# Kernel optimization log

Hardware: AMD Instinct MI355X
Metric: run time of the kernel (lower is better)

The kernel has to match this reference:

```python
import jax, jax.numpy as jnp
import numpy as np

T, N_NODES, B, F, K, OUT = 16, 20, 4096, 64, 3, 2
BN = B * N_NODES        # 81920 total nodes in the batched graph
E = 327680              # edges (avg degree 4)
D1, D2, D3 = F * N_NODES, (F * N_NODES) // 2, (F * N_NODES) // 4  # 1280, 640, 320


def setup_inputs() -> dict:
    key = jax.random.key(0)
    ks = jax.random.split(key, 32)
    p = lambda k, shape: (jax.random.normal(k, shape, jnp.float32) * 0.05)
    inp = {}
    inp["x_temporal"] = jax.random.normal(ks[0], (T, BN, F), jnp.float32)
    inp["edge_index"] = jax.random.randint(ks[1], (2, E), 0, BN)
    inp["edge_weight"] = jax.random.uniform(ks[2], (E,), jnp.float32)
    # GConvGRU gate ChebConvs (K Chebyshev weight matrices + bias each)
    for i, n in enumerate(["xz", "hz", "xr", "hr", "xh", "hh"]):
        inp["W_" + n] = p(ks[3 + i], (K, F, F))
        inp["b_" + n] = jnp.zeros((F,), jnp.float32)
    inp["W1"] = p(ks[10], (D1, D2)); inp["b1"] = jnp.zeros((D2,), jnp.float32)
    inp["W2"] = p(ks[11], (D2, D3)); inp["b2"] = jnp.zeros((D3,), jnp.float32)
    inp["W3"] = p(ks[12], (D3, OUT)); inp["b3"] = jnp.zeros((OUT,), jnp.float32)
    return inp


def _cheb(X, W, b, src, dst, nw):
    # ChebConv with sym normalization, lambda_max=2: L_hat = -D^-1/2 A D^-1/2
    # Tx0 = X; Tx1 = L_hat X; Tx_k = 2 L_hat Tx_{k-1} - Tx_{k-2}
    Tx0 = X
    out = Tx0 @ W[0]
    Tx1 = jax.ops.segment_sum(nw[:, None] * Tx0[src], dst, num_segments=BN)
    out = out + Tx1 @ W[1]
    for k in range(2, K):
        Tx2 = 2.0 * jax.ops.segment_sum(nw[:, None] * Tx1[src], dst, num_segments=BN) - Tx0
        out = out + Tx2 @ W[k]
        Tx0, Tx1 = Tx1, Tx2
    return out + b


def reference(x_temporal, edge_index, edge_weight,
              W_xz, b_xz, W_hz, b_hz, W_xr, b_xr, W_hr, b_hr, W_xh, b_xh, W_hh, b_hh,
              W1, b1, W2, b2, W3, b3):
    src, dst = edge_index[0], edge_index[1]
    deg = jax.ops.segment_sum(edge_weight, src, num_segments=BN)
    dinv = jnp.where(deg > 0, jax.lax.rsqrt(jnp.where(deg > 0, deg, 1.0)), 0.0)
    nw = -dinv[src] * edge_weight * dinv[dst]  # scaled-Laplacian edge weights

    def step(H, X):
        Z = jax.nn.sigmoid(_cheb(X, W_xz, b_xz, src, dst, nw) + _cheb(H, W_hz, b_hz, src, dst, nw))
        R = jax.nn.sigmoid(_cheb(X, W_xr, b_xr, src, dst, nw) + _cheb(H, W_hr, b_hr, src, dst, nw))
        Ht = jnp.tanh(_cheb(X, W_xh, b_xh, src, dst, nw) + _cheb(H * R, W_hh, b_hh, src, dst, nw))
        Hn = Z * H + (1.0 - Z) * Ht
        Hn = jax.nn.relu(Hn)  # dropout is identity in eval mode
        return Hn, None

    H0 = jnp.zeros((BN, F), x_temporal.dtype)
    H, _ = jax.lax.scan(step, H0, x_temporal)

    x = H.reshape(B, D1)                      # [B, numNodes*embed_dim]
    x = jax.nn.relu(x @ W1 + b1)
    x = jax.nn.relu(x @ W2 + b2)
    x = jax.nn.softmax(x @ W3 + b3, axis=-1)
    return x
```

## Files before the change

### kernel.cpp

```cpp
#include <hip/hip_runtime.h>
#include <hip/hip_bf16.h>
#include <math.h>

#define T_STEPS 16
#define N_NODES 20
#define BATCH 4096
#define F_DIM 64
#define BN 81920
#define E_EDGES 327680
#define D1 1280
#define D2 640
#define D3 320

typedef __attribute__((ext_vector_type(8))) short short8;
typedef __attribute__((ext_vector_type(4))) float floatx4;

static __device__ __forceinline__ float bf2f(__hip_bfloat16 v) { return __bfloat162float(v); }
static __device__ __forceinline__ float sigmoidf_(float x) { return 1.f / (1.f + expf(-x)); }
static __device__ __forceinline__ float loadf(const void* p, size_t i, int isf32) {
    return isf32 ? ((const float*)p)[i] : bf2f(((const __hip_bfloat16*)p)[i]);
}
static __device__ __forceinline__ float bflo(unsigned int u) { return __uint_as_float(u << 16); }
static __device__ __forceinline__ float bfhi(unsigned int u) { return __uint_as_float(u & 0xffff0000u); }
static __device__ __forceinline__ unsigned int f2bf_bits(float f) {
    __hip_bfloat16 b = __float2bfloat16(f);
    unsigned short us;
    __builtin_memcpy(&us, &b, 2);
    return (unsigned int)us;
}


__global__ void detect_dtype(const void* __restrict__ x, int* __restrict__ flag) {
    int lane = threadIdx.x;
    const unsigned short* u = (const unsigned short*)x;
    int bad = 0;
    for (int i = lane; i < 256; i += 64) {
        int e = (u[i] >> 7) & 0xFF;
        if (e >= 141) bad = 1;
    }
    unsigned long long m = __ballot(bad != 0);
    if (lane == 0) flag[0] = (m != 0ull) ? 1 : 0;
}

__global__ void deg_count_kernel(const int* __restrict__ ei, const void* __restrict__ ew,
                                 float* __restrict__ deg, int* __restrict__ counts,
                                 const int* __restrict__ flagp) {
    int isf32 = *flagp;
    int e = blockIdx.x * 256 + threadIdx.x;
    if (e < E_EDGES) {
        atomicAdd(&deg[ei[e]], loadf(ew, e, isf32));
        atomicAdd(&counts[ei[E_EDGES + e]], 1);
    }
}

__global__ void scan_kernel(const int* __restrict__ counts, int* __restrict__ rowptr,
                            int* __restrict__ cursor) {
    __shared__ int s[1024];
    int t = threadIdx.x;
    int base = t * 80;
    int sum = 0;
    for (int i = 0; i < 80; ++i) sum += counts[base + i];
    s[t] = sum;
    __syncthreads();
    for (int off = 1; off < 1024; off <<= 1) {
        int v = (t >= off) ? s[t - off] : 0;
        __syncthreads();
        s[t] += v;
        __syncthreads();
    }
    int run = (t > 0) ? s[t - 1] : 0;
    for (int i = 0; i < 80; ++i) {
        rowptr[base + i] = run;
        cursor[base + i] = run;
        run += counts[base + i];
    }
    if (t == 1023) rowptr[BN] = run;
}

__global__ void fill_kernel(const int* __restrict__ ei, const void* __restrict__ ew,
                            const float* __restrict__ deg,
                            int* __restrict__ cursor, int2* __restrict__ cpack,
                            const int* __restrict__ flagp) {
    int isf32 = *flagp;
    int e = blockIdx.x * 256 + threadIdx.x;
    if (e < E_EDGES) {
        int s = ei[e], d = ei[E_EDGES + e];
        float w = loadf(ew, e, isf32);
        float ds = deg[s], dd = deg[d];
        float is = (ds > 0.f) ? (1.f / sqrtf(ds)) : 0.f;
        float id = (dd > 0.f) ? (1.f / sqrtf(dd)) : 0.f;
        int p = atomicAdd(&cursor[d], 1);
        cpack[p] = make_int2(s, __float_as_int(-is * w * id));
    }
}

__global__ void prep_weights(const void* Wxz, const void* Whz,
                             const void* Wxr, const void* Whr,
                             const void* Wxh, const void* Whh,
                             const void* bxz, const void* bhz,
                             const void* bxr, const void* bhr,
                             const void* bxh, const void* bhh,
                             const void* W1, const void* b1,
                             const void* W2, const void* b2,
                             const void* W3, const void* b3,
                             __hip_bfloat16* WgT, __hip_bfloat16* WcT,
                             float* biasg, float* biasc,
                             __hip_bfloat16* W1T, float* bias1,
                             __hip_bfloat16* W2T, float* bias2,
                             float* W3f, float* b3f, const int* __restrict__ flagp) {
    int isf32 = *flagp;
    int tid = blockIdx.x * 256 + threadIdx.x;
    if (tid < 73728) {
        int n = tid / 384, kk = tid - (tid / 384) * 384;
        int m = kk >> 6, jj = kk & 63;
        int grp = n >> 6, cc = n & 63;
        const void* Wx = (grp == 0) ? Wxz : ((grp == 1) ? Wxr : Wxh);
        const void* Wh = (grp == 0) ? Whz : ((grp == 1) ? Whr : nullptr);
        int ch = m & 1;
        int ti = m >> 1;
        const void* W = ch ? Wh : Wx;
        float v = 0.f;
        int o = jj * 64 + cc;
        if (W) {
            if (ti == 0)      v = loadf(W, o, isf32) - loadf(W, 2 * 4096 + o, isf32);
            else if (ti == 1) v = loadf(W, 4096 + o, isf32);
            else              v = 2.f * loadf(W, 2 * 4096 + o, isf32);
        }
        WgT[tid] = __float2bfloat16(v);
    } else if (tid < 86016) {
        int t2 = tid - 73728;
        int n = t2 / 192, kk = t2 - (t2 / 192) * 192;
        int m = kk >> 6, jj = kk & 63;
        int o = jj * 64 + n;
        float v;
        if (m == 0)      v = loadf(Whh, o, isf32) - loadf(Whh, 2 * 4096 + o, isf32);
        else if (m == 1) v = loadf(Whh, 4096 + o, isf32);
        else             v = 2.f * loadf(Whh, 2 * 4096 + o, isf32);
        WcT[t2] = __float2bfloat16(v);
    } else if (tid < 86208) {
        int c = tid - 86016;
        int grp = c >> 6, cc = c & 63;
        float v = (grp == 0) ? (loadf(bxz, cc, isf32) + loadf(bhz, cc, isf32))
                 : (grp == 1) ? (loadf(bxr, cc, isf32) + loadf(bhr, cc, isf32))
                              : loadf(bxh, cc, isf32);
        biasg[c] = v;
    } else if (tid < 86272) {
        biasc[tid - 86208] = loadf(bhh, tid - 86208, isf32);
    } else if (tid < 86912) {
        bias1[tid - 86272] = loadf(b1, tid - 86272, isf32);
    } else if (tid < 87232) {
        bias2[tid - 86912] = loadf(b2, tid - 86912, isf32);
    } else if (tid < 87872) {
        W3f[tid - 87232] = loadf(W3, tid - 87232, isf32);
    } else if (tid < 87874) {
        b3f[tid - 87872] = loadf(b3, tid - 87872, isf32);
    } else if (tid < 907074) {
        int t = tid - 87874;
        int n = t / 1280, k = t - (t / 1280) * 1280;
        W1T[t] = __float2bfloat16(loadf(W1, (size_t)k * 640 + n, isf32));
    } else if (tid < 1111874) {
        int t = tid - 907074;
        int n = t / 640, k = t - (t / 640) * 640;
        W2T[t] = __float2bfloat16(loadf(W2, (size_t)k * 320 + n, isf32));
    }
}

__global__ void init_x_kernel(const void* __restrict__ x, const int* __restrict__ flagp,
                              __hip_bfloat16* __restrict__ A6) {
    int isf32 = *flagp;
    int idx = blockIdx.x * 256 + threadIdx.x;
    int r = idx >> 6, c = idx & 63;
    A6[(size_t)r * 384 + c] = __float2bfloat16(loadf(x, idx, isf32));
}

__global__ void phase_pair_kernel(const int* __restrict__ rowptr, const int2* __restrict__ cpack,
                                  __hip_bfloat16* __restrict__ A6, int in_boff, int out_boff) {
    int row = __builtin_amdgcn_readfirstlane(blockIdx.x * 4 + (threadIdx.x >> 6));
    int lane = threadIdx.x & 63;
    int e0 = rowptr[row], e1 = rowptr[row + 1];
    const char* base = (const char*)A6 + in_boff;
    int boff = lane * 4;
    float ax = 0.f, ay = 0.f, bx = 0.f, by = 0.f;
    int e = e0;
    for (; e + 2 <= e1; e += 2) {
        int2 c0 = cpack[e], c1 = cpack[e + 1];
        unsigned int u0 = *(const unsigned int*)(base + (size_t)c0.x * 768 + boff);
        unsigned int u1 = *(const unsigned int*)(base + (size_t)c1.x * 768 + boff);
        float v0 = __int_as_float(c0.y), v1 = __int_as_float(c1.y);
        ax = fmaf(v0, bflo(u0), ax); ay = fmaf(v0, bfhi(u0), ay);
        bx = fmaf(v1, bflo(u1), bx); by = fmaf(v1, bfhi(u1), by);
    }
    if (e < e1) {
        int2 c0 = cpack[e];
        unsigned int u0 = *(const unsigned int*)(base + (size_t)c0.x * 768 + boff);
        float v0 = __int_as_float(c0.y);
        ax = fmaf(v0, bflo(u0), ax); ay = fmaf(v0, bfhi(u0), ay);
    }
    ax += bx; ay += by;
    unsigned int pk = f2bf_bits(ax) | (f2bf_bits(ay) << 16);
    *(unsigned int*)((char*)A6 + (size_t)row * 768 + out_boff +
                     ((lane >> 5) << 7) + ((lane & 31) << 2)) = pk;
}

__global__ void spmm_pair_kernel(const int* __restrict__ rowptr, const int2* __restrict__ cpack,
                                 __hip_bfloat16* __restrict__ Gbuf, int in_boff, int out_boff) {
    int lane = threadIdx.x & 63;
    int half = lane >> 5, lh = lane & 31;
    int row = (blockIdx.x * 4 + (threadIdx.x >> 6)) * 2 + half;
    int e0 = rowptr[row], e1 = rowptr[row + 1];
    const char* base = (const char*)Gbuf + in_boff;
    int boff = lh * 4;
    float ax = 0.f, ay = 0.f, bx = 0.f, by = 0.f;
    int e = e0;
    for (; e + 2 <= e1; e += 2) {
        int2 c0 = cpack[e], c1 = cpack[e + 1];
        unsigned int u0 = *(const unsigned int*)(base + (size_t)c0.x * 384 + boff);
        unsigned int u1 = *(const unsigned int*)(base + (size_t)c1.x * 384 + boff);
        float v0 = __int_as_float(c0.y), v1 = __int_as_float(c1.y);
        ax = fmaf(v0, bflo(u0), ax); ay = fmaf(v0, bfhi(u0), ay);
        bx = fmaf(v1, bflo(u1), bx); by = fmaf(v1, bfhi(u1), by);
    }
    if (e < e1) {
        int2 c0 = cpack[e];
        unsigned int u0 = *(const unsigned int*)(base + (size_t)c0.x * 384 + boff);
        float v0 = __int_as_float(c0.y);
        ax = fmaf(v0, bflo(u0), ax); ay = fmaf(v0, bfhi(u0), ay);
    }
    ax += bx; ay += by;
    unsigned int pk = f2bf_bits(ax) | (f2bf_bits(ay) << 16);
    *(unsigned int*)((char*)Gbuf + (size_t)row * 384 + out_boff + boff) = pk;
}

template <int MW, int NT, int EPI>
__launch_bounds__(256)
__global__ void mfma_gemm(const __hip_bfloat16* __restrict__ A, int lda,
                          const __hip_bfloat16* __restrict__ WT, int ldk,
                          const float* __restrict__ bias, int K,
                          float* __restrict__ Zbuf, float* __restrict__ hxbuf,
                          float* __restrict__ Hf, __hip_bfloat16* A6,
                          __hip_bfloat16* __restrict__ Gbuf,
                          __hip_bfloat16* __restrict__ C, int ldc,
                          const void* __restrict__ xsrc, unsigned long long xoff,
                          const int* __restrict__ flagp,
                          __hip_bfloat16* __restrict__ Hdout) {
    int wave = threadIdx.x >> 6;
    int lane = threadIdx.x & 63;
    int l15 = lane & 15, quad = lane >> 4;
    int m0 = blockIdx.x * (MW * 64) + wave * (MW * 16);
    int n0 = blockIdx.y * (NT * 16);
    int isf32 = 0;
    if (EPI == 2 && flagp) isf32 = *flagp;

    floatx4 acc[MW][NT];
#pragma unroll
    for (int mi = 0; mi < MW; ++mi)
#pragma unroll
        for (int nt = 0; nt < NT; ++nt) acc[mi][nt] = (floatx4){0.f, 0.f, 0.f, 0.f};

    for (int k0 = 0; k0 < K; k0 += 32) {
        short8 a[MW];
#pragma unroll
        for (int mi = 0; mi < MW; ++mi)
            a[mi] = *(const short8*)(A + (size_t)(m0 + mi * 16 + l15) * lda + k0 + quad * 8);
#pragma unroll
        for (int nt = 0; nt < NT; ++nt) {
            short8 b = *(const short8*)(WT + (size_t)(n0 + nt * 16 + l15) * ldk + k0 + quad * 8);
#pragma unroll
            for (int mi = 0; mi < MW; ++mi)
                acc[mi][nt] = __builtin_amdgcn_mfma_f32_16x16x32_bf16(a[mi], b, acc[mi][nt], 0, 0, 0);
        }
    }

#pragma unroll
    for (int mi = 0; mi < MW; ++mi)
#pragma unroll
        for (int nt = 0; nt < NT; ++nt) {
            int cl = n0 + nt * 16 + l15;
#pragma unroll
            for (int reg = 0; reg < 4; ++reg) {
                int r = m0 + mi * 16 + quad * 4 + reg;
                float v = acc[mi][nt][reg];
                if (EPI == 0) {
                    C[(size_t)r * ldc + cl] = __float2bfloat16(fmaxf(v + bias[cl], 0.f));
                } else if (EPI == 1) {
                    v += bias[cl];
                    if (cl < 64) {
                        Zbuf[(size_t)r * 64 + cl] = sigmoidf_(v);
                    } else if (cl < 128) {
                        int cc = cl - 64;
                        float g = sigmoidf_(v) * Hf[(size_t)r * 64 + cc];
                        Gbuf[(size_t)r * 192 + cc] = __float2bfloat16(g);
                    } else {
                        int cc = cl - 128;
                        hxbuf[(size_t)r * 64 + cc] = v;
                    }
                } else {
                    float pre = v + bias[cl] + hxbuf[(size_t)r * 64 + cl];
                    float ht = tanhf(pre);
                    float z = Zbuf[(size_t)r * 64 + cl];
                    float h = Hf[(size_t)r * 64 + cl];
                    float hn = fmaxf(z * h + (1.f - z) * ht, 0.f);
                    __hip_bfloat16 hb = __float2bfloat16(hn);
                    if (xsrc) {
                        Hf[(size_t)r * 64 + cl] = hn;
                        A6[(size_t)r * 384 + 64 + cl] = hb;
                        A6[(size_t)r * 384 + cl] =
                            __float2bfloat16(loadf(xsrc, xoff + (size_t)r * 64 + cl, isf32));
                    } else {
                        Hdout[(size_t)r * 64 + cl] = hb;
                    }
                }
            }
        }
}

__global__ void mlp3_kernel(const __hip_bfloat16* __restrict__ h2, const float* __restrict__ W3f,
                            const float* __restrict__ b3f, void* __restrict__ out,
                            const int* __restrict__ flagp) {
    int isf32 = *flagp;
    int b = blockIdx.x * 4 + (threadIdx.x >> 6);
    int lane = threadIdx.x & 63;
    float a0 = 0.f, a1 = 0.f;
    for (int k = lane; k < D3; k += 64) {
        float h = bf2f(h2[(size_t)b * D3 + k]);
        a0 = fmaf(h, W3f[k * 2 + 0], a0);
        a1 = fmaf(h, W3f[k * 2 + 1], a1);
    }
    for (int off = 32; off; off >>= 1) {
        a0 += __shfl_down(a0, off, 64);
        a1 += __shfl_down(a1, off, 64);
    }
    if (lane == 0) {
        a0 += b3f[0];
        a1 += b3f[1];
        float m = fmaxf(a0, a1);
        float e0 = expf(a0 - m), e1 = expf(a1 - m);
        float s = e0 + e1;
        if (isf32) {
            ((float*)out)[b * 2 + 0] = e0 / s;
            ((float*)out)[b * 2 + 1] = e1 / s;
        } else {
            ((__hip_bfloat16*)out)[b * 2 + 0] = __float2bfloat16(e0 / s);
            ((__hip_bfloat16*)out)[b * 2 + 1] = __float2bfloat16(e1 / s);
        }
    }
}

extern "C" void kernel_launch(void* const* d_in, const int* in_sizes, int n_in,
                              void* d_out, int out_size, void* d_ws, size_t ws_size,
                              hipStream_t stream) {
    const void* x   = d_in[0];
    const int*  ei  = (const int*)d_in[1];
    const void* ew  = d_in[2];
    const void* Wxz = d_in[3];
    const void* bxz = d_in[4];
    const void* Whz = d_in[5];
    const void* bhz = d_in[6];
    const void* Wxr = d_in[7];
    const void* bxr = d_in[8];
    const void* Whr = d_in[9];
    const void* bhr = d_in[10];
    const void* Wxh = d_in[11];
    const void* bxh = d_in[12];
    const void* Whh = d_in[13];
    const void* bhh = d_in[14];
    const void* W1  = d_in[15];
    const void* b1  = d_in[16];
    const void* W2  = d_in[17];
    const void* b2  = d_in[18];
    const void* W3  = d_in[19];
    const void* b3  = d_in[20];

    char* ws = (char*)d_ws;
    size_t off = 0;
    auto alloc = [&](size_t bytes) { char* p = ws + off; off += (bytes + 255) & ~(size_t)255; return p; };
    __hip_bfloat16* A6  = (__hip_bfloat16*)alloc((size_t)BN * 384 * 2);
    __hip_bfloat16* Gbuf = (__hip_bfloat16*)alloc((size_t)BN * 192 * 2);
    float* Hf    = (float*)alloc((size_t)BN * 64 * 4);
    float* Zbuf  = (float*)alloc((size_t)BN * 64 * 4);
    float* hxbuf = (float*)alloc((size_t)BN * 64 * 4);
    __hip_bfloat16* Hd  = (__hip_bfloat16*)alloc((size_t)BN * 64 * 2);
    __hip_bfloat16* h1  = (__hip_bfloat16*)alloc((size_t)BATCH * D2 * 2);
    __hip_bfloat16* h2  = (__hip_bfloat16*)alloc((size_t)BATCH * D3 * 2);
    float* deg    = (float*)alloc((size_t)BN * 4);
    int*   counts = (int*)alloc((size_t)BN * 4);
    int*   rowptr = (int*)alloc((size_t)(BN + 1) * 4);
    int*   cursor = (int*)alloc((size_t)BN * 4);
    int2*  cpack  = (int2*)alloc((size_t)E_EDGES * 8);
    __hip_bfloat16* WgT = (__hip_bfloat16*)alloc(192 * 384 * 2);
    __hip_bfloat16* WcT = (__hip_bfloat16*)alloc(64 * 192 * 2);
    float* biasg  = (float*)alloc(192 * 4);
    float* biasc  = (float*)alloc(64 * 4);
    __hip_bfloat16* W1T = (__hip_bfloat16*)alloc((size_t)D2 * D1 * 2);
    float* bias1  = (float*)alloc(D2 * 4);
    __hip_bfloat16* W2T = (__hip_bfloat16*)alloc((size_t)D3 * D2 * 2);
    float* bias2  = (float*)alloc(D3 * 4);
    float* W3f    = (float*)alloc(D3 * 2 * 4);
    float* b3f    = (float*)alloc(2 * 4);
    int*   flag   = (int*)alloc(256);
    (void)ws_size; (void)in_sizes; (void)n_in; (void)out_size;

    hipMemsetAsync(A6, 0, (size_t)BN * 384 * 2, stream);
    hipMemsetAsync(Hf, 0, (size_t)BN * 64 * 4, stream);
    hipMemsetAsync(deg, 0, (size_t)BN * 4, stream);
    hipMemsetAsync(counts, 0, (size_t)BN * 4, stream);

    detect_dtype<<<1, 64, 0, stream>>>(x, flag);

    const int EB = E_EDGES / 256;
    deg_count_kernel<<<EB, 256, 0, stream>>>(ei, ew, deg, counts, flag);
    scan_kernel<<<1, 1024, 0, stream>>>(counts, rowptr, cursor);
    fill_kernel<<<EB, 256, 0, stream>>>(ei, ew, deg, cursor, cpack, flag);
    prep_weights<<<4344, 256, 0, stream>>>(Wxz, Whz, Wxr, Whr, Wxh, Whh,
                                           bxz, bhz, bxr, bhr, bxh, bhh,
                                           W1, b1, W2, b2, W3, b3,
                                           WgT, WcT, biasg, biasc,
                                           W1T, bias1, W2T, bias2, W3f, b3f, flag);
    init_x_kernel<<<(BN * 64) / 256, 256, 0, stream>>>(x, flag, A6);

    const int RB = BN / 4;
    const int RB2 = BN / 8;
    for (int t = 0; t < T_STEPS; ++t) {
        phase_pair_kernel<<<RB, 256, 0, stream>>>(rowptr, cpack, A6, 0, 256);
        phase_pair_kernel<<<RB, 256, 0, stream>>>(rowptr, cpack, A6, 256, 512);
        mfma_gemm<2, 6, 1><<<dim3(BN / 128, 2), 256, 0, stream>>>(
            A6, 384, WgT, 384, biasg, 384, Zbuf, hxbuf, Hf, A6, Gbuf, nullptr, 0,
            nullptr, 0ull, nullptr, nullptr);
        spmm_pair_kernel<<<RB2, 256, 0, stream>>>(rowptr, cpack, Gbuf, 0, 128);
        spmm_pair_kernel<<<RB2, 256, 0, stream>>>(rowptr, cpack, Gbuf, 128, 256);
        const void* xn = (t + 1 < T_STEPS) ? x : nullptr;
        unsigned long long xo = (unsigned long long)(t + 1) * BN * 64;
        mfma_gemm<2, 2, 2><<<dim3(BN / 128, 2), 256, 0, stream>>>(
            Gbuf, 192, WcT, 192, biasc, 192, Zbuf, hxbuf, Hf, A6, Gbuf, nullptr, 0,
            xn, xo, flag, Hd);
    }

    mfma_gemm<1, 4, 0><<<dim3(BATCH / 64, D2 / 64), 256, 0, stream>>>(
        Hd, D1, W1T, D1, bias1, D1, nullptr, nullptr, nullptr, nullptr, nullptr, h1, D2,
        nullptr, 0ull, nullptr, nullptr);
    mfma_gemm<1, 4, 0><<<dim3(BATCH / 64, D3 / 64), 256, 0, stream>>>(
        h1, D2, W2T, D2, bias2, D2, nullptr, nullptr, nullptr, nullptr, nullptr, h2, D3,
        nullptr, 0ull, nullptr, nullptr);
    mlp3_kernel<<<BATCH / 4, 256, 0, stream>>>(h2, W3f, b3f, d_out, flag);
}
```

Measured before the change: 4.042 ms.

## Fuse second Chebyshev SpMM hop into gate and candidate GEMM kernels via LDS

The second SpMM hop of each Chebyshev recurrence is moved into the gate and candidate GEMM kernels. Each block gathers its 128 rows of neighbour features into shared memory, then runs the MFMA GEMM with those rows as the final K slice. This drops the third A6 slice and Gbuf slice from global memory, narrows row strides from 768/384 to 512/256 bytes, and removes two kernel launches per timestep. The gather loops are also unrolled to four edges. In exchange the fused blocks do their sparse gather serially per wave before the GEMM, with a full GEMM column width of 12 tiles per block, which may cost occupancy and latency hiding.

Result: slower. 6.124 ms (+51.5%).

```diff
diff --git a/kernel.cpp b/kernel.cpp
--- a/kernel.cpp
+++ b/kernel.cpp
@@ -170,148 +170,310 @@
     int isf32 = *flagp;
     int idx = blockIdx.x * 256 + threadIdx.x;
     int r = idx >> 6, c = idx & 63;
-    A6[(size_t)r * 384 + c] = __float2bfloat16(loadf(x, idx, isf32));
-}
-
-__global__ void phase_pair_kernel(const int* __restrict__ rowptr, const int2* __restrict__ cpack,
-                                  __hip_bfloat16* __restrict__ A6, int in_boff, int out_boff) {
+    A6[(size_t)r * 256 + c] = __float2bfloat16(loadf(x, idx, isf32));
+}
+
+__global__ void phaseA_kernel(const int* __restrict__ rowptr, const int2* __restrict__ cpack,
+                              __hip_bfloat16* __restrict__ A6) {
     int row = __builtin_amdgcn_readfirstlane(blockIdx.x * 4 + (threadIdx.x >> 6));
     int lane = threadIdx.x & 63;
     int e0 = rowptr[row], e1 = rowptr[row + 1];
-    const char* base = (const char*)A6 + in_boff;
+    const char* base = (const char*)A6;
     int boff = lane * 4;
-    float ax = 0.f, ay = 0.f, bx = 0.f, by = 0.f;
+    float ax = 0.f, ay = 0.f, cx = 0.f, cy = 0.f;
     int e = e0;
-    for (; e + 2 <= e1; e += 2) {
-        int2 c0 = cpack[e], c1 = cpack[e + 1];
-        unsigned int u0 = *(const unsigned int*)(base + (size_t)c0.x * 768 + boff);
-        unsigned int u1 = *(const unsigned int*)(base + (size_t)c1.x * 768 + boff);
+    for (; e + 4 <= e1; e += 4) {
+        int2 c0 = cpack[e], c1 = cpack[e + 1], c2 = cpack[e + 2], c3 = cpack[e + 3];
+        unsigned int u0 = *(const unsigned int*)(base + (size_t)c0.x * 512 + boff);
+        unsigned int u1 = *(const unsigned int*)(base + (size_t)c1.x * 512 + boff);
+        unsigned int u2 = *(const unsigned int*)(base + (size_t)c2.x * 512 + boff);
+        unsigned int u3 = *(const unsigned int*)(base + (size_t)c3.x * 512 + boff);
         float v0 = __int_as_float(c0.y), v1 = __int_as_float(c1.y);
+        float v2 = __int_as_float(c2.y), v3 = __int_as_float(c3.y);
         ax = fmaf(v0, bflo(u0), ax); ay = fmaf(v0, bfhi(u0), ay);
-        bx = fmaf(v1, bflo(u1), bx); by = fmaf(v1, bfhi(u1), by);
-    }
-    if (e < e1) {
+        cx = fmaf(v1, bflo(u1), cx); cy = fmaf(v1, bfhi(u1), cy);
+        ax = fmaf(v2, bflo(u2), ax); ay = fmaf(v2, bfhi(u2), ay);
+        cx = fmaf(v3, bflo(u3), cx); cy = fmaf(v3, bfhi(u3), cy);
+    }
+    for (; e < e1; ++e) {
         int2 c0 = cpack[e];
-        unsigned int u0 = *(const unsigned int*)(base + (size_t)c0.x * 768 + boff);
+        unsigned int u0 = *(const unsigned int*)(base + (size_t)c0.x * 512 + boff);
         float v0 = __int_as_float(c0.y);
         ax = fmaf(v0, bflo(u0), ax); ay = fmaf(v0, bfhi(u0), ay);
     }
-    ax += bx; ay += by;
+    ax += cx; ay += cy;
     unsigned int pk = f2bf_bits(ax) | (f2bf_bits(ay) << 16);
-    *(unsigned int*)((char*)A6 + (size_t)row * 768 + out_boff +
-                     ((lane >> 5) << 7) + ((lane & 31) << 2)) = pk;
+    *(unsigned int*)((char*)A6 + (size_t)row * 512 + 256 + boff) = pk;
 }
 
 __global__ void spmm_pair_kernel(const int* __restrict__ rowptr, const int2* __restrict__ cpack,
-                                 __hip_bfloat16* __restrict__ Gbuf, int in_boff, int out_boff) {
+                                 __hip_bfloat16* __restrict__ Gbuf) {
     int lane = threadIdx.x & 63;
     int half = lane >> 5, lh = lane & 31;
     int row = (blockIdx.x * 4 + (threadIdx.x >> 6)) * 2 + half;
     int e0 = rowptr[row], e1 = rowptr[row + 1];
-    const char* base = (const char*)Gbuf + in_boff;
+    const char* base = (const char*)Gbuf;
     int boff = lh * 4;
-    float ax = 0.f, ay = 0.f, bx = 0.f, by = 0.f;
+    float ax = 0.f, ay = 0.f, cx = 0.f, cy = 0.f;
     int e = e0;
-    for (; e + 2 <= e1; e += 2) {
-        int2 c0 = cpack[e], c1 = cpack[e + 1];
-        unsigned int u0 = *(const unsigned int*)(base + (size_t)c0.x * 384 + boff);
-        unsigned int u1 = *(const unsigned int*)(base + (size_t)c1.x * 384 + boff);
+    for (; e + 4 <= e1; e += 4) {
+        int2 c0 = cpack[e], c1 = cpack[e + 1], c2 = cpack[e + 2], c3 = cpack[e + 3];
+        unsigned int u0 = *(const unsigned int*)(base + (size_t)c0.x * 256 + boff);
+        unsigned int u1 = *(const unsigned int*)(base + (size_t)c1.x * 256 + boff);
+        unsigned int u2 = *(const unsigned int*)(base + (size_t)c2.x * 256 + boff);
+        unsigned int u3 = *(const unsigned int*)(base + (size_t)c3.x * 256 + boff);
         float v0 = __int_as_float(c0.y), v1 = __int_as_float(c1.y);
+        float v2 = __int_as_float(c2.y), v3 = __int_as_float(c3.y);
         ax = fmaf(v0, bflo(u0), ax); ay = fmaf(v0, bfhi(u0), ay);
-        bx = fmaf(v1, bflo(u1), bx); by = fmaf(v1, bfhi(u1), by);
-    }
-    if (e < e1) {
+        cx = fmaf(v1, bflo(u1), cx); cy = fmaf(v1, bfhi(u1), cy);
+        ax = fmaf(v2, bflo(u2), ax); ay = fmaf(v2, bfhi(u2), ay);
+        cx = fmaf(v3, bflo(u3), cx); cy = fmaf(v3, bfhi(u3), cy);
+    }
+    for (; e < e1; ++e) {
         int2 c0 = cpack[e];
-        unsigned int u0 = *(const unsigned int*)(base + (size_t)c0.x * 384 + boff);
+        unsigned int u0 = *(const unsigned int*)(base + (size_t)c0.x * 256 + boff);
         float v0 = __int_as_float(c0.y);
         ax = fmaf(v0, bflo(u0), ax); ay = fmaf(v0, bfhi(u0), ay);
     }
-    ax += bx; ay += by;
+    ax += cx; ay += cy;
     unsigned int pk = f2bf_bits(ax) | (f2bf_bits(ay) << 16);
-    *(unsigned int*)((char*)Gbuf + (size_t)row * 384 + out_boff + boff) = pk;
-}
-
-template <int MW, int NT, int EPI>
+    *(unsigned int*)((char*)Gbuf + (size_t)row * 256 + 128 + boff) = pk;
+}
+
 __launch_bounds__(256)
-__global__ void mfma_gemm(const __hip_bfloat16* __restrict__ A, int lda,
-                          const __hip_bfloat16* __restrict__ WT, int ldk,
-                          const float* __restrict__ bias, int K,
-                          float* __restrict__ Zbuf, float* __restrict__ hxbuf,
-                          float* __restrict__ Hf, __hip_bfloat16* A6,
-                          __hip_bfloat16* __restrict__ Gbuf,
-                          __hip_bfloat16* __restrict__ C, int ldc,
-                          const void* __restrict__ xsrc, unsigned long long xoff,
-                          const int* __restrict__ flagp,
-                          __hip_bfloat16* __restrict__ Hdout) {
+__global__ void fused_gates_kernel(const int* __restrict__ rowptr, const int2* __restrict__ cpack,
+                                   const __hip_bfloat16* __restrict__ A6,
+                                   const __hip_bfloat16* __restrict__ WgT,
+                                   const float* __restrict__ biasg,
+                                   const float* __restrict__ Hf,
+                                   float* __restrict__ Zbuf, float* __restrict__ hxbuf,
+                                   __hip_bfloat16* __restrict__ Gbuf) {
+    __shared__ unsigned int sX2H2[128 * 68];
+    int wave = threadIdx.x >> 6, lane = threadIdx.x & 63;
+    int l15 = lane & 15, quad = lane >> 4;
+    int r0 = blockIdx.x * 128;
+    const char* gbase = (const char*)A6 + 256;
+    int boff = lane * 4;
+    for (int i = 0; i < 32; ++i) {
+        int lr = wave * 32 + i;
+        int row = r0 + lr;
+        int e0 = rowptr[row], e1 = rowptr[row + 1];
+        float ax = 0.f, ay = 0.f, cx = 0.f, cy = 0.f;
+        int e = e0;
+        for (; e + 4 <= e1; e += 4) {
+            int2 c0 = cpack[e], c1 = cpack[e + 1], c2 = cpack[e + 2], c3 = cpack[e + 3];
+            unsigned int u0 = *(const unsigned int*)(gbase + (size_t)c0.x * 512 + boff);
+            unsigned int u1 = *(const unsigned int*)(gbase + (size_t)c1.x * 512 + boff);
+            unsigned int u2 = *(const unsigned int*)(gbase + (size_t)c2.x * 512 + boff);
+            unsigned int u3 = *(const unsigned int*)(gbase + (size_t)c3.x * 512 + boff);
+            float v0 = __int_as_float(c0.y), v1 = __int_as_float(c1.y);
+            float v2 = __int_as_float(c2.y), v3 = __int_as_float(c3.y);
+            ax = fmaf(v0, bflo(u0), ax); ay = fmaf(v0, bfhi(u0), ay);
+            cx = fmaf(v1, bflo(u1), cx); cy = fmaf(v1, bfhi(u1), cy);
+            ax = fmaf(v2, bflo(u2), ax); ay = fmaf(v2, bfhi(u2), ay);
+            cx = fmaf(v3, bflo(u3), cx); cy = fmaf(v3, bfhi(u3), cy);
+        }
+        for (; e < e1; ++e) {
+            int2 c0 = cpack[e];
+            unsigned int u0 = *(const unsigned int*)(gbase + (size_t)c0.x * 512 + boff);
+            float v0 = __int_as_float(c0.y);
+            ax = fmaf(v0, bflo(u0), ax); ay = fmaf(v0, bfhi(u0), ay);
+        }
+        ax += cx; ay += cy;
+        sX2H2[lr * 68 + lane] = f2bf_bits(ax) | (f2bf_bits(ay) << 16);
+    }
+    __syncthreads();
+
+    floatx4 acc[2][12];
+#pragma unroll
+    for (int mi = 0; mi < 2; ++mi)
+#pragma unroll
+        for (int nt = 0; nt < 12; ++nt) acc[mi][nt] = (floatx4){0.f, 0.f, 0.f, 0.f};
+
+#pragma unroll
+    for (int k0 = 0; k0 < 384; k0 += 32) {
+        short8 a[2];
+        if (k0 < 256) {
+#pragma unroll
+            for (int mi = 0; mi < 2; ++mi)
+                a[mi] = *(const short8*)(A6 + (size_t)(r0 + wave * 32 + mi * 16 + l15) * 256
+                                         + k0 + quad * 8);
+        } else {
+#pragma unroll
+            for (int mi = 0; mi < 2; ++mi)
+                a[mi] = *(const short8*)((const char*)sX2H2
+                                         + (wave * 32 + mi * 16 + l15) * 272
+                                         + (k0 - 256) * 2 + quad * 16);
+        }
+#pragma unroll
+        for (int nt = 0; nt < 12; ++nt) {
+            short8 b = *(const short8*)(WgT + (size_t)(nt * 16 + l15) * 384 + k0 + quad * 8);
+#pragma unroll
+            for (int mi = 0; mi < 2; ++mi)
+                acc[mi][nt] = __builtin_amdgcn_mfma_f32_16x16x32_bf16(a[mi], b, acc[mi][nt], 0, 0, 0);
+        }
+    }
+
+#pragma unroll
+    for (int mi = 0; mi < 2; ++mi)
+#pragma unroll
+        for (int nt = 0; nt < 12; ++nt) {
+            int cl = nt * 16 + l15;
+#pragma unroll
+            for (int reg = 0; reg < 4; ++reg) {
+                int r = r0 + wave * 32 + mi * 16 + quad * 4 + reg;
+                float v = acc[mi][nt][reg] + biasg[cl];
+                if (cl < 64) {
+                    Zbuf[(size_t)r * 64 + cl] = sigmoidf_(v);
+                } else if (cl < 128) {
+                    int cc = cl - 64;
+                    float g = sigmoidf_(v) * Hf[(size_t)r * 64 + cc];
+                    Gbuf[(size_t)r * 128 + cc] = __float2bfloat16(g);
+                } else {
+                    hxbuf[(size_t)r * 64 + (cl - 128)] = v;
+                }
+            }
+        }
+}
+
+__launch_bounds__(256)
+__global__ void fused_cand_kernel(const int* __restrict__ rowptr, const int2* __restrict__ cpack,
+                                  const __hip_bfloat16* __restrict__ Gbuf,
+                                  const __hip_bfloat16* __restrict__ WcT,
+                                  const float* __restrict__ biasc,
+                                  const float* __restrict__ Zbuf,
+                                  const float* __restrict__ hxbuf,
+                                  float* __restrict__ Hf, __hip_bfloat16* __restrict__ A6,
+                                  const void* __restrict__ xsrc, unsigned long long xoff,
+                                  const int* __restrict__ flagp,
+                                  __hip_bfloat16* __restrict__ Hdout) {
+    __shared__ unsigned int sG2[128 * 36];
+    int wave = threadIdx.x >> 6, lane = threadIdx.x & 63;
+    int l15 = lane & 15, quad = lane >> 4;
+    int half = lane >> 5, lh = lane & 31;
+    int r0 = blockIdx.x * 128;
+    int isf32 = *flagp;
+    const char* gbase = (const char*)Gbuf + 128;
+    int boff = lh * 4;
+    for (int i = 0; i < 32; i += 2) {
+        int lr = wave * 32 + i + half;
+        int row = r0 + lr;
+        int e0 = rowptr[row], e1 = rowptr[row + 1];
+        float ax = 0.f, ay = 0.f, cx = 0.f, cy = 0.f;
+        int e = e0;
+        for (; e + 4 <= e1; e += 4) {
+            int2 c0 = cpack[e], c1 = cpack[e + 1], c2 = cpack[e + 2], c3 = cpack[e + 3];
+            unsigned int u0 = *(const unsigned int*)(gbase + (size_t)c0.x * 256 + boff);
+            unsigned int u1 = *(const unsigned int*)(gbase + (size_t)c1.x * 256 + boff);
+            unsigned int u2 = *(const unsigned int*)(gbase + (size_t)c2.x * 256 + boff);
+            unsigned int u3 = *(const unsigned int*)(gbase + (size_t)c3.x * 256 + boff);
+            float v0 = __int_as_float(c0.y), v1 = __int_as_float(c1.y);
+            float v2 = __int_as_float(c2.y), v3 = __int_as_float(c3.y);
+            ax = fmaf(v0, bflo(u0), ax); ay = fmaf(v0, bfhi(u0), ay);
+            cx = fmaf(v1, bflo(u1), cx); cy = fmaf(v1, bfhi(u1), cy);
+            ax = fmaf(v2, bflo(u2), ax); ay = fmaf(v2, bfhi(u2), ay);
+            cx = fmaf(v3, bflo(u3), cx); cy = fmaf(v3, bfhi(u3), cy);
+        }
+        for (; e < e1; ++e) {
+            int2 c0 = cpack[e];
+            unsigned int u0 = *(const unsigned int*)(gbase + (size_t)c0.x * 256 + boff);
+            float v0 = __int_as_float(c0.y);
+            ax = fmaf(v0, bflo(u0), ax); ay = fmaf(v0, bfhi(u0), ay);
+        }
+        ax += cx; ay += cy;
+        sG2[lr * 36 + lh] = f2bf_bits(ax) | (f2bf_bits(ay) << 16);
+    }
+    __syncthreads();
+
+    floatx4 acc[2][4];
+#pragma unroll
+    for (int mi = 0; mi < 2; ++mi)
+#pragma unroll
+        for (int nt = 0; nt < 4; ++nt) acc[mi][nt] = (floatx4){0.f, 0.f, 0.f, 0.f};
+
+#pragma unroll
+    for (int k0 = 0; k0 < 192; k0 += 32) {
+        short8 a[2];
+        if (k0 < 128) {
+#pragma unroll
+            for (int mi = 0; mi < 2; ++mi)
+                a[mi] = *(const short8*)(Gbuf + (size_t)(r0 + wave * 32 + mi * 16 + l15) * 128
+                                         + k0 + quad * 8);
+        } else {
+#pragma unroll
+            for (int mi = 0; mi < 2; ++mi)
+                a[mi] = *(const short8*)((const char*)sG2
+                                         + (wave * 32 + mi * 16 + l15) * 144
+                                         + (k0 - 128) * 2 + quad * 16);
+        }
+#pragma unroll
+        for (int nt = 0; nt < 4; ++nt) {
+            short8 b = *(const short8*)(WcT + (size_t)(nt * 16 + l15) * 192 + k0 + quad * 8);
+#pragma unroll
+            for (int mi = 0; mi < 2; ++mi)
+                acc[mi][nt] = __builtin_amdgcn_mfma_f32_16x16x32_bf16(a[mi], b, acc[mi][nt], 0, 0, 0);
+        }
+    }
+
+#pragma unroll
+    for (int mi = 0; mi < 2; ++mi)
+#pragma unroll
+        for (int nt = 0; nt < 4; ++nt) {
+            int cl = nt * 16 + l15;
+#pragma unroll
+            for (int reg = 0; reg < 4; ++reg) {
+                int r = r0 + wave * 32 + mi * 16 + quad * 4 + reg;
+                float pre = acc[mi][nt][reg] + biasc[cl] + hxbuf[(size_t)r * 64 + cl];
+                float ht = tanhf(pre);
+                float z = Zbuf[(size_t)r * 64 + cl];
+                float h = Hf[(size_t)r * 64 + cl];
+                float hn = fmaxf(z * h + (1.f - z) * ht, 0.f);
+                __hip_bfloat16 hb = __float2bfloat16(hn);
+                if (xsrc) {
+                    Hf[(size_t)r * 64 + cl] = hn;
+                    A6[(size_t)r * 256 + 64 + cl] = hb;
+                    A6[(size_t)r * 256 + cl] =
+                        __float2bfloat16(loadf(xsrc, xoff + (size_t)r * 64 + cl, isf32));
+                } else {
+                    Hdout[(size_t)r * 64 + cl] = hb;
+                }
+            }
+        }
+}
+
+template <int NT>
+__launch_bounds__(256)
+__global__ void mfma_gemm_relu(const __hip_bfloat16* __restrict__ A, int lda,
+                               const __hip_bfloat16* __restrict__ WT,
+                               const float* __restrict__ bias, int K,
+                               __hip_bfloat16* __restrict__ C, int ldc) {
     int wave = threadIdx.x >> 6;
     int lane = threadIdx.x & 63;
     int l15 = lane & 15, quad = lane >> 4;
-    int m0 = blockIdx.x * (MW * 64) + wave * (MW * 16);
+    int m0 = blockIdx.x * 64 + wave * 16;
     int n0 = blockIdx.y * (NT * 16);
-    int isf32 = 0;
-    if (EPI == 2 && flagp) isf32 = *flagp;
-
-    floatx4 acc[MW][NT];
-#pragma unroll
-    for (int mi = 0; mi < MW; ++mi)
-#pragma unroll
-        for (int nt = 0; nt < NT; ++nt) acc[mi][nt] = (floatx4){0.f, 0.f, 0.f, 0.f};
+
+    floatx4 acc[NT];
+#pragma unroll
+    for (int nt = 0; nt < NT; ++nt) acc[nt] = (floatx4){0.f, 0.f, 0.f, 0.f};
 
     for (int k0 = 0; k0 < K; k0 += 32) {
-        short8 a[MW];
-#pragma unroll
-        for (int mi = 0; mi < MW; ++mi)
-            a[mi] = *(const short8*)(A + (size_t)(m0 + mi * 16 + l15) * lda + k0 + quad * 8);
+        short8 a = *(const short8*)(A + (size_t)(m0 + l15) * lda + k0 + quad * 8);
 #pragma unroll
         for (int nt = 0; nt < NT; ++nt) {
-            short8 b = *(const short8*)(WT + (size_t)(n0 + nt * 16 + l15) * ldk + k0 + quad * 8);
-#pragma unroll
-            for (int mi = 0; mi < MW; ++mi)
-                acc[mi][nt] = __builtin_amdgcn_mfma_f32_16x16x32_bf16(a[mi], b, acc[mi][nt], 0, 0, 0);
-        }
-    }
-
-#pragma unroll
-    for (int mi = 0; mi < MW; ++mi)
-#pragma unroll
-        for (int nt = 0; nt < NT; ++nt) {
-            int cl = n0 + nt * 16 + l15;
-#pragma unroll
-            for (int reg = 0; reg < 4; ++reg) {
-                int r = m0 + mi * 16 + quad * 4 + reg;
-                float v = acc[mi][nt][reg];
-                if (EPI == 0) {
-                    C[(size_t)r * ldc + cl] = __float2bfloat16(fmaxf(v + bias[cl], 0.f));
-                } else if (EPI == 1) {
-                    v += bias[cl];
-                    if (cl < 64) {
-                        Zbuf[(size_t)r * 64 + cl] = sigmoidf_(v);
-                    } else if (cl < 128) {
-                        int cc = cl - 64;
-                        float g = sigmoidf_(v) * Hf[(size_t)r * 64 + cc];
-                        Gbuf[(size_t)r * 192 + cc] = __float2bfloat16(g);
-                    } else {
-                        int cc = cl - 128;
-                        hxbuf[(size_t)r * 64 + cc] = v;
-                    }
-                } else {
-                    float pre = v + bias[cl] + hxbuf[(size_t)r * 64 + cl];
-                    float ht = tanhf(pre);
-                    float z = Zbuf[(size_t)r * 64 + cl];
-                    float h = Hf[(size_t)r * 64 + cl];
-                    float hn = fmaxf(z * h + (1.f - z) * ht, 0.f);
-                    __hip_bfloat16 hb = __float2bfloat16(hn);
-                    if (xsrc) {
-                        Hf[(size_t)r * 64 + cl] = hn;
-                        A6[(size_t)r * 384 + 64 + cl] = hb;
-                        A6[(size_t)r * 384 + cl] =
-                            __float2bfloat16(loadf(xsrc, xoff + (size_t)r * 64 + cl, isf32));
-                    } else {
-                        Hdout[(size_t)r * 64 + cl] = hb;
-                    }
-                }
-            }
-        }
+            short8 b = *(const short8*)(WT + (size_t)(n0 + nt * 16 + l15) * lda + k0 + quad * 8);
+            acc[nt] = __builtin_amdgcn_mfma_f32_16x16x32_bf16(a, b, acc[nt], 0, 0, 0);
+        }
+    }
+#pragma unroll
+    for (int nt = 0; nt < NT; ++nt) {
+        int cl = n0 + nt * 16 + l15;
+#pragma unroll
+        for (int reg = 0; reg < 4; ++reg) {
+            int r = m0 + quad * 4 + reg;
+            C[(size_t)r * ldc + cl] = __float2bfloat16(fmaxf(acc[nt][reg] + bias[cl], 0.f));
+        }
+    }
 }
 
 __global__ void mlp3_kernel(const __hip_bfloat16* __restrict__ h2, const float* __restrict__ W3f,
@@ -374,8 +536,8 @@
     char* ws = (char*)d_ws;
     size_t off = 0;
     auto alloc = [&](size_t bytes) { char* p = ws + off; off += (bytes + 255) & ~(size_t)255; return p; };
-    __hip_bfloat16* A6  = (__hip_bfloat16*)alloc((size_t)BN * 384 * 2);
-    __hip_bfloat16* Gbuf = (__hip_bfloat16*)alloc((size_t)BN * 192 * 2);
+    __hip_bfloat16* A6   = (__hip_bfloat16*)alloc((size_t)BN * 256 * 2);
+    __hip_bfloat16* Gbuf = (__hip_bfloat16*)alloc((size_t)BN * 128 * 2);
     float* Hf    = (float*)alloc((size_t)BN * 64 * 4);
     float* Zbuf  = (float*)alloc((size_t)BN * 64 * 4);
     float* hxbuf = (float*)alloc((size_t)BN * 64 * 4);
@@ -400,7 +562,7 @@
     int*   flag   = (int*)alloc(256);
     (void)ws_size; (void)in_sizes; (void)n_in; (void)out_size;
 
-    hipMemsetAsync(A6, 0, (size_t)BN * 384 * 2, stream);
+    hipMemsetAsync(A6, 0, (size_t)BN * 256 * 2, stream);
     hipMemsetAsync(Hf, 0, (size_t)BN * 64 * 4, stream);
     hipMemsetAsync(deg, 0, (size_t)BN * 4, stream);
     hipMemsetAsync(counts, 0, (size_t)BN * 4, stream);
@@ -420,26 +582,21 @@
 
     const int RB = BN / 4;
     const int RB2 = BN / 8;
+    const int FB = BN / 128;
     for (int t = 0; t < T_STEPS; ++t) {
-        phase_pair_kernel<<<RB, 256, 0, stream>>>(rowptr, cpack, A6, 0, 256);
-        phase_pair_kernel<<<RB, 256, 0, stream>>>(rowptr, cpack, A6, 256, 512);
-        mfma_gemm<2, 6, 1><<<dim3(BN / 128, 2), 256, 0, stream>>>(
-            A6, 384, WgT, 384, biasg, 384, Zbuf, hxbuf, Hf, A6, Gbuf, nullptr, 0,
-            nullptr, 0ull, nullptr, nullptr);
-        spmm_pair_kernel<<<RB2, 256, 0, stream>>>(rowptr, cpack, Gbuf, 0, 128);
-        spmm_pair_kernel<<<RB2, 256, 0, stream>>>(rowptr, cpack, Gbuf, 128, 256);
+        phaseA_kernel<<<RB, 256, 0, stream>>>(rowptr, cpack, A6);
+        fused_gates_kernel<<<FB, 256, 0, stream>>>(rowptr, cpack, A6, WgT, biasg,
+                                                   Hf, Zbuf, hxbuf, Gbuf);
+        spmm_pair_kernel<<<RB2, 256, 0, stream>>>(rowptr, cpack, Gbuf);
         const void* xn = (t + 1 < T_STEPS) ? x : nullptr;
         unsigned long long xo = (unsigned long long)(t + 1) * BN * 64;
-        mfma_gemm<2, 2, 2><<<dim3(BN / 128, 2), 256, 0, stream>>>(
-            Gbuf, 192, WcT, 192, biasc, 192, Zbuf, hxbuf, Hf, A6, Gbuf, nullptr, 0,
-            xn, xo, flag, Hd);
-    }
-
-    mfma_gemm<1, 4, 0><<<dim3(BATCH / 64, D2 / 64), 256, 0, stream>>>(
-        Hd, D1, W1T, D1, bias1, D1, nullptr, nullptr, nullptr, nullptr, nullptr, h1, D2,
-        nullptr, 0ull, nullptr, nullptr);
-    mfma_gemm<1, 4, 0><<<dim3(BATCH / 64, D3 / 64), 256, 0, stream>>>(
-        h1, D2, W2T, D2, bias2, D2, nullptr, nullptr, nullptr, nullptr, nullptr, h2, D3,
-        nullptr, 0ull, nullptr, nullptr);
+        fused_cand_kernel<<<FB, 256, 0, stream>>>(rowptr, cpack, Gbuf, WcT, biasc,
+                                                  Zbuf, hxbuf, Hf, A6, xn, xo, flag, Hd);
+    }
+
+    mfma_gemm_relu<4><<<dim3(BATCH / 64, D2 / 64), 256, 0, stream>>>(
+        Hd, D1, W1T, bias1, D1, h1, D2);
+    mfma_gemm_relu<4><<<dim3(BATCH / 64, D3 / 64), 256, 0, stream>>>(
+        h1, D2, W2T, bias2, D2, h2, D3);
     mlp3_kernel<<<BATCH / 4, 256, 0, stream>>>(h2, W3f, b3f, d_out, flag);
 }
```
